# Kernel optimization log

Hardware: AMD Instinct MI355X
Metric: run time of the kernel (lower is better)

The kernel has to match this reference:

```python
import jax, jax.numpy as jnp
import numpy as np

B, N, M, L, H = 32, 4096, 256, 128, 4
GAMMA = 2.0


def setup_inputs() -> dict:
    key = jax.random.key(0)
    kx, km, kv, ku, kw = jax.random.split(key, 5)
    x = jax.random.normal(kx, (B, N, M), dtype=jnp.float32)
    masks = (jax.random.uniform(km, (B, N)) > 0.3).astype(jnp.float32)
    # VarianceScaling(scale=0.1, fan_in, uniform) ~ small init; exact dist doesn't affect math
    V = jax.random.normal(kv, (H, M, L), dtype=jnp.float32) * 0.02
    U = jax.random.normal(ku, (H, M, L), dtype=jnp.float32) * 0.02
    w = jax.random.normal(kw, (H, L, 1), dtype=jnp.float32) * 0.05
    return {"x": x, "masks": masks, "V": V, "U": U, "w": w}


def reference(x, masks, V, U, w):
    # x: [B,N,M], masks: [B,N], V/U: [H,M,L], w: [H,L,1]
    m = masks[:, None, :, None]  # [B,1,N,1] broadcast over heads
    gated = jnp.tanh(jnp.einsum('bnm,hml->bhnl', x, V)) * jax.nn.sigmoid(
        jnp.einsum('bnm,hml->bhnl', x, U))          # [B,H,N,L]
    logits = jnp.einsum('bhnl,hl->bhn', gated, w[..., 0])[..., None]  # [B,H,N,1]
    a = m * logits                                   # masked logits (as in original)
    a = m * jnp.exp(a)                               # masked exp
    a = a / jnp.sum(a, axis=2, keepdims=True)        # softmax over instances
    ag = a ** GAMMA
    a = ag / jnp.sum(ag, axis=2, keepdims=True)      # gamma-power renorm
    emb = jnp.einsum('bhnk,bnm->bhm', a, x)          # weighted sum; k is the trailing 1
    emb = emb.reshape(B, H * M)                      # concat heads along axis=1
    att = jnp.transpose(a, (1, 0, 2, 3))             # [H,B,N,1] (per-head attention list)
    return (att, emb)
```

## Files before the change

### kernel.cpp

```cpp
#include <hip/hip_runtime.h>
#include <hip/hip_bf16.h>
#include <stdint.h>

#define B_ 32
#define N_ 4096
#define M_ 256
#define L_ 128
#define H_ 4
#define BN_ (B_ * N_)

typedef __bf16 bf16x8 __attribute__((ext_vector_type(8)));
typedef float  f32x4  __attribute__((ext_vector_type(4)));

__device__ __forceinline__ unsigned short f2bf(float f) {
    unsigned int u = __float_as_uint(f);
    u += 0x7fffu + ((u >> 16) & 1u);
    return (unsigned short)(u >> 16);
}
__device__ __forceinline__ unsigned int pack2(float lo, float hi) {
    return (unsigned int)f2bf(lo) | ((unsigned int)f2bf(hi) << 16);
}

__global__ void prep_vu(const float* __restrict__ V, const float* __restrict__ U,
                        unsigned short* __restrict__ Vt, unsigned short* __restrict__ Ut) {
    int idx = blockIdx.x * 256 + threadIdx.x;
    int m = idx & (M_ - 1);
    int l = (idx >> 8) & (L_ - 1);
    int h = idx >> 15;
    Vt[idx] = f2bf(V[((size_t)h * M_ + m) * L_ + l]);
    Ut[idx] = f2bf(U[((size_t)h * M_ + m) * L_ + l]);
}

#define BM 128
#define BK 64

__global__ __launch_bounds__(256, 2)
void gemm_logits(const float* __restrict__ x,
                 const unsigned short* __restrict__ Vt,
                 const unsigned short* __restrict__ Ut,
                 const float* __restrict__ w,
                 float* __restrict__ logits) {
    __shared__ __align__(16) unsigned short xs[BM * BK];
    __shared__ __align__(16) unsigned short vs[L_ * BK];
    __shared__ __align__(16) unsigned short us[L_ * BK];
    __shared__ float wl[L_];

    const int h    = blockIdx.x >> 10;
    const int tile = blockIdx.x & 1023;
    const int row0 = tile * BM;
    const int tid  = threadIdx.x;
    const int lane = tid & 63;
    const int wave = tid >> 6;

    if (tid < L_) wl[tid] = w[h * L_ + tid];

    f32x4 accV[2][8], accU[2][8];
#pragma unroll
    for (int rf = 0; rf < 2; ++rf)
#pragma unroll
        for (int cf = 0; cf < 8; ++cf) {
            accV[rf][cf] = (f32x4){0.f, 0.f, 0.f, 0.f};
            accU[rf][cf] = (f32x4){0.f, 0.f, 0.f, 0.f};
        }

    const unsigned short* Vh = Vt + (size_t)h * L_ * M_;
    const unsigned short* Uh = Ut + (size_t)h * L_ * M_;

    const int g = lane >> 4;
    const int c = lane & 15;

    for (int ks = 0; ks < 4; ++ks) {
        const int k0 = ks * BK;
        __syncthreads();

#pragma unroll
        for (int p = 0; p < 4; ++p) {
            int row = p * 32 + (tid >> 3);
            int kk  = (tid & 7) * 8;
            const float* gx = x + (size_t)(row0 + row) * M_ + k0 + kk;
            float4 a = *(const float4*)gx;
            float4 b = *(const float4*)(gx + 4);
            uint4 o;
            o.x = pack2(a.x, a.y); o.y = pack2(a.z, a.w);
            o.z = pack2(b.x, b.y); o.w = pack2(b.z, b.w);
            int byte = (row * BK + kk) * 2;
            byte ^= (row & 7) << 4;
            *(uint4*)((char*)xs + byte) = o;
        }
#pragma unroll
        for (int p = 0; p < 4; ++p) {
            int l  = p * 32 + (tid >> 3);
            int kk = (tid & 7) * 8;
            uint4 v = *(const uint4*)(Vh + (size_t)l * M_ + k0 + kk);
            uint4 u = *(const uint4*)(Uh + (size_t)l * M_ + k0 + kk);
            int byte = (l * BK + kk) * 2;
            byte ^= (l & 7) << 4;
            *(uint4*)((char*)vs + byte) = v;
            *(uint4*)((char*)us + byte) = u;
        }
        __syncthreads();

#pragma unroll
        for (int ksub = 0; ksub < 2; ++ksub) {
            bf16x8 afr[2];
#pragma unroll
            for (int rf = 0; rf < 2; ++rf) {
                int row = wave * 32 + rf * 16 + c;
                int byte = (row * BK + ksub * 32 + g * 8) * 2;
                byte ^= (row & 7) << 4;
                afr[rf] = *(const bf16x8*)((const char*)xs + byte);
            }
#pragma unroll
            for (int cf = 0; cf < 8; ++cf) {
                int l = cf * 16 + c;
                int byte = (l * BK + ksub * 32 + g * 8) * 2;
                byte ^= (l & 7) << 4;
                bf16x8 bv = *(const bf16x8*)((const char*)vs + byte);
                bf16x8 bu = *(const bf16x8*)((const char*)us + byte);
#pragma unroll
                for (int rf = 0; rf < 2; ++rf) {
                    accV[rf][cf] = __builtin_amdgcn_mfma_f32_16x16x32_bf16(afr[rf], bv, accV[rf][cf], 0, 0, 0);
                    accU[rf][cf] = __builtin_amdgcn_mfma_f32_16x16x32_bf16(afr[rf], bu, accU[rf][cf], 0, 0, 0);
                }
            }
        }
    }

#pragma unroll
    for (int rf = 0; rf < 2; ++rf) {
        float plog[4] = {0.f, 0.f, 0.f, 0.f};
#pragma unroll
        for (int cf = 0; cf < 8; ++cf) {
            float wv = wl[cf * 16 + c];
#pragma unroll
            for (int i = 0; i < 4; ++i) {
                float vv = accV[rf][cf][i];
                float uu = accU[rf][cf][i];
                vv = fminf(fmaxf(vv, -20.f), 20.f);
                float e2v = __expf(2.f * vv);
                float t = __fdividef(e2v - 1.f, e2v + 1.f);
                float s = __fdividef(1.f, 1.f + __expf(-uu));
                plog[i] += t * s * wv;
            }
        }
#pragma unroll
        for (int i = 0; i < 4; ++i) {
            float v = plog[i];
            v += __shfl_xor(v, 1);
            v += __shfl_xor(v, 2);
            v += __shfl_xor(v, 4);
            v += __shfl_xor(v, 8);
            if (c == 0) {
                int rowflat = row0 + wave * 32 + rf * 16 + g * 4 + i;
                int b = rowflat >> 12;
                int n = rowflat & (N_ - 1);
                logits[((size_t)b * H_ + h) * N_ + n] = v;
            }
        }
    }
}

__global__ __launch_bounds__(256)
void softmax_att(const float* __restrict__ logits, const float* __restrict__ masks,
                 float* __restrict__ att) {
    const int bh = blockIdx.x;
    const int b = bh >> 2, h = bh & 3;
    __shared__ float e2s[N_];
    __shared__ float red[4];
    const int tid = threadIdx.x;

    float sum = 0.f;
#pragma unroll
    for (int i = 0; i < N_ / 256; ++i) {
        int n = i * 256 + tid;
        float lg = logits[((size_t)b * H_ + h) * N_ + n];
        float mv = masks[(size_t)b * N_ + n];
        float e = mv * __expf(mv * lg);
        float e2 = e * e;
        e2s[n] = e2;
        sum += e2;
    }
#pragma unroll
    for (int off = 32; off >= 1; off >>= 1) sum += __shfl_xor(sum, off);
    if ((tid & 63) == 0) red[tid >> 6] = sum;
    __syncthreads();
    float S = red[0] + red[1] + red[2] + red[3];
    float inv = 1.f / S;
#pragma unroll
    for (int i = 0; i < N_ / 256; ++i) {
        int n = i * 256 + tid;
        att[((size_t)h * B_ + b) * N_ + n] = e2s[n] * inv;
    }
}

#define NCH 32
#define CHUNK (N_ / NCH)

__global__ __launch_bounds__(256)
void emb_partial(const float* __restrict__ x, const float* __restrict__ att,
                 float* __restrict__ part) {
    const int bc = blockIdx.x;
    const int b = bc >> 5, ch = bc & 31;
    __shared__ float as[H_][CHUNK];
    const int tid = threadIdx.x;

    for (int i = tid; i < H_ * CHUNK; i += 256) {
        int hh = i >> 7;
        int j  = i & (CHUNK - 1);
        as[hh][j] = att[((size_t)hh * B_ + b) * N_ + ch * CHUNK + j];
    }
    __syncthreads();

    float a0 = 0.f, a1 = 0.f, a2 = 0.f, a3 = 0.f;
    const float* xp = x + ((size_t)b * N_ + ch * CHUNK) * M_ + tid;
#pragma unroll 4
    for (int j = 0; j < CHUNK; ++j) {
        float xv = xp[(size_t)j * M_];
        a0 += as[0][j] * xv;
        a1 += as[1][j] * xv;
        a2 += as[2][j] * xv;
        a3 += as[3][j] * xv;
    }
    float* pp = part + (size_t)bc * H_ * M_ + tid;
    pp[0 * M_] = a0; pp[1 * M_] = a1; pp[2 * M_] = a2; pp[3 * M_] = a3;
}

__global__ __launch_bounds__(256)
void emb_reduce(const float* __restrict__ part, float* __restrict__ emb) {
    int idx = blockIdx.x * 256 + threadIdx.x;
    int b = idx >> 10;
    int r = idx & 1023;
    float s = 0.f;
#pragma unroll
    for (int ci = 0; ci < NCH; ++ci)
        s += part[((size_t)(b * NCH + ci)) * (H_ * M_) + r];
    emb[idx] = s;
}

extern "C" void kernel_launch(void* const* d_in, const int* in_sizes, int n_in,
                              void* d_out, int out_size, void* d_ws, size_t ws_size,
                              hipStream_t stream) {
    const float* x     = (const float*)d_in[0];
    const float* masks = (const float*)d_in[1];
    const float* V     = (const float*)d_in[2];
    const float* U     = (const float*)d_in[3];
    const float* w     = (const float*)d_in[4];

    float* att = (float*)d_out;
    float* emb = att + (size_t)H_ * B_ * N_;

    char* ws = (char*)d_ws;
    unsigned short* Vt = (unsigned short*)ws;
    unsigned short* Ut = (unsigned short*)(ws + 262144);
    float* logits      = (float*)(ws + 524288);
    float* part        = (float*)(ws + 524288 + 2097152);

    prep_vu   <<<(H_ * L_ * M_) / 256, 256, 0, stream>>>(V, U, Vt, Ut);
    gemm_logits<<<(BN_ / BM) * H_,      256, 0, stream>>>(x, Vt, Ut, w, logits);
    softmax_att<<<B_ * H_,              256, 0, stream>>>(logits, masks, att);
    emb_partial<<<B_ * NCH,             256, 0, stream>>>(x, att, part);
    emb_reduce <<<(B_ * H_ * M_) / 256, 256, 0, stream>>>(part, emb);
}
```

Baseline: 186.9 us.

## Pre-convert x to swizzled bf16 tiles and stream them into LDS

```diff
diff --git a/kernel.cpp b/kernel.cpp
--- a/kernel.cpp
+++ b/kernel.cpp
@@ -11,6 +11,7 @@
 
 typedef __bf16 bf16x8 __attribute__((ext_vector_type(8)));
 typedef float  f32x4  __attribute__((ext_vector_type(4)));
+typedef float  f32x16 __attribute__((ext_vector_type(16)));
 
 __device__ __forceinline__ unsigned short f2bf(float f) {
     unsigned int u = __float_as_uint(f);
@@ -21,8 +22,197 @@
     return (unsigned int)f2bf(lo) | ((unsigned int)f2bf(hi) << 16);
 }
 
-__global__ void prep_vu(const float* __restrict__ V, const float* __restrict__ U,
-                        unsigned short* __restrict__ Vt, unsigned short* __restrict__ Ut) {
+__device__ __forceinline__ void gload16(const void* g, void* l) {
+    __builtin_amdgcn_global_load_lds(
+        (const __attribute__((address_space(1))) unsigned int*)g,
+        (__attribute__((address_space(3))) unsigned int*)l, 16, 0, 0);
+}
+
+__global__ void prep_x(const float* __restrict__ x, unsigned short* __restrict__ xb) {
+    const int blk  = blockIdx.x;
+    const int tile = blk >> 2, ks = blk & 3;
+    const int i    = threadIdx.x;
+    const int kk   = (i & 7) * 8;
+    char* dst = (char*)xb + (size_t)blk * 16384;
+#pragma unroll
+    for (int rep = 0; rep < 4; ++rep) {
+        int row = rep * 32 + (i >> 3);
+        const float* gx = x + (size_t)(tile * 128 + row) * M_ + ks * 64 + kk;
+        float4 a = *(const float4*)gx;
+        float4 b = *(const float4*)(gx + 4);
+        uint4 o;
+        o.x = pack2(a.x, a.y); o.y = pack2(a.z, a.w);
+        o.z = pack2(b.x, b.y); o.w = pack2(b.z, b.w);
+        int byte = (row * 64 + kk) * 2;
+        byte ^= (row & 7) << 4;
+        *(uint4*)(dst + byte) = o;
+    }
+}
+
+__global__ void prep_vu_img(const float* __restrict__ V, const float* __restrict__ U,
+                            unsigned short* __restrict__ vu) {
+    __shared__ float slab[64][129];
+    const int b   = blockIdx.x;
+    const int mat = b & 1, ks = (b >> 1) & 3, h = b >> 3;
+    const float* src = (mat ? U : V) + ((size_t)h * M_ + ks * 64) * L_;
+    const int tid = threadIdx.x;
+#pragma unroll
+    for (int rep = 0; rep < 32; ++rep) {
+        int idx = rep * 256 + tid;
+        slab[idx >> 7][idx & 127] = src[(size_t)(idx >> 7) * L_ + (idx & 127)];
+    }
+    __syncthreads();
+    char* dst = (char*)vu + (size_t)b * 16384;
+#pragma unroll
+    for (int rep = 0; rep < 4; ++rep) {
+        int cidx = rep * 256 + tid;
+        int l  = cidx >> 3;
+        int kk = (cidx & 7) * 8;
+        uint4 o;
+        o.x = pack2(slab[kk + 0][l], slab[kk + 1][l]);
+        o.y = pack2(slab[kk + 2][l], slab[kk + 3][l]);
+        o.z = pack2(slab[kk + 4][l], slab[kk + 5][l]);
+        o.w = pack2(slab[kk + 6][l], slab[kk + 7][l]);
+        int byte = (l * 64 + kk) * 2;
+        byte ^= (l & 7) << 4;
+        *(uint4*)(dst + byte) = o;
+    }
+}
+
+__global__ __launch_bounds__(256, 2)
+void gemm_fast(const unsigned short* __restrict__ xb,
+               const unsigned short* __restrict__ vu,
+               const float* __restrict__ w,
+               float* __restrict__ logits) {
+    __shared__ __align__(16) unsigned short xs[8192];
+    __shared__ __align__(16) unsigned short vs[8192];
+    __shared__ __align__(16) unsigned short us[8192];
+    __shared__ float wl[L_];
+    __shared__ float part[2][128];
+
+    const int orig    = blockIdx.x;
+    const int logical = (orig & 7) * 512 + (orig >> 3);
+    const int tile    = logical >> 2;
+    const int h       = logical & 3;
+
+    const int tid  = threadIdx.x;
+    const int lane = tid & 63;
+    const int wv   = tid >> 6;
+    const int cc   = lane & 31;
+    const int hi   = lane >> 5;
+    const int r0   = (wv & 1) * 64;
+    const int L0   = (wv >> 1) * 64;
+
+    if (tid < L_) wl[tid] = w[h * L_ + tid];
+
+    f32x16 accV[2][2], accU[2][2];
+#pragma unroll
+    for (int rf = 0; rf < 2; ++rf)
+#pragma unroll
+        for (int j = 0; j < 2; ++j) {
+            accV[rf][j] = (f32x16)(0.f);
+            accU[rf][j] = (f32x16)(0.f);
+        }
+
+    const char* xsrc0 = (const char*)xb + (size_t)tile * 4 * 16384;
+    const char* vusrc = (const char*)vu + (size_t)h * 4 * 32768;
+
+    for (int ks = 0; ks < 4; ++ks) {
+        if (ks) __syncthreads();
+        const char* xsrc = xsrc0 + ks * 16384;
+        const char* vsrc = vusrc + ks * 32768;
+        const char* usrc = vsrc + 16384;
+#pragma unroll
+        for (int j = 0; j < 4; ++j) {
+            int off = (wv * 4 + j) * 1024;
+            gload16(xsrc + off + lane * 16, (char*)xs + off);
+            gload16(vsrc + off + lane * 16, (char*)vs + off);
+            gload16(usrc + off + lane * 16, (char*)us + off);
+        }
+        __syncthreads();
+
+#pragma unroll
+        for (int ksub = 0; ksub < 4; ++ksub) {
+            const int kb = ksub * 32 + hi * 16;
+            bf16x8 a0, a1, bv0, bv1, bu0, bu1;
+            {
+                int r = r0 + cc;
+                int byte = (r * 128 + kb) ^ ((r & 7) << 4);
+                a0 = *(const bf16x8*)((const char*)xs + byte);
+                r = r0 + 32 + cc;
+                byte = (r * 128 + kb) ^ ((r & 7) << 4);
+                a1 = *(const bf16x8*)((const char*)xs + byte);
+                int l = L0 + cc;
+                byte = (l * 128 + kb) ^ ((l & 7) << 4);
+                bv0 = *(const bf16x8*)((const char*)vs + byte);
+                bu0 = *(const bf16x8*)((const char*)us + byte);
+                l = L0 + 32 + cc;
+                byte = (l * 128 + kb) ^ ((l & 7) << 4);
+                bv1 = *(const bf16x8*)((const char*)vs + byte);
+                bu1 = *(const bf16x8*)((const char*)us + byte);
+            }
+            accV[0][0] = __builtin_amdgcn_mfma_f32_32x32x16_bf16(a0, bv0, accV[0][0], 0, 0, 0);
+            accV[0][1] = __builtin_amdgcn_mfma_f32_32x32x16_bf16(a0, bv1, accV[0][1], 0, 0, 0);
+            accU[0][0] = __builtin_amdgcn_mfma_f32_32x32x16_bf16(a0, bu0, accU[0][0], 0, 0, 0);
+            accU[0][1] = __builtin_amdgcn_mfma_f32_32x32x16_bf16(a0, bu1, accU[0][1], 0, 0, 0);
+            accV[1][0] = __builtin_amdgcn_mfma_f32_32x32x16_bf16(a1, bv0, accV[1][0], 0, 0, 0);
+            accV[1][1] = __builtin_amdgcn_mfma_f32_32x32x16_bf16(a1, bv1, accV[1][1], 0, 0, 0);
+            accU[1][0] = __builtin_amdgcn_mfma_f32_32x32x16_bf16(a1, bu0, accU[1][0], 0, 0, 0);
+            accU[1][1] = __builtin_amdgcn_mfma_f32_32x32x16_bf16(a1, bu1, accU[1][1], 0, 0, 0);
+        }
+    }
+
+    const float w0 = wl[L0 + cc];
+    const float w1 = wl[L0 + 32 + cc];
+    float p[32];
+#pragma unroll
+    for (int rf = 0; rf < 2; ++rf)
+#pragma unroll
+        for (int i = 0; i < 16; ++i) {
+            float s = 0.f;
+#pragma unroll
+            for (int j = 0; j < 2; ++j) {
+                float vv = accV[rf][j][i];
+                float uu = accU[rf][j][i];
+                vv = fminf(fmaxf(vv, -20.f), 20.f);
+                float A = __expf(2.f * vv);
+                float E = __expf(fminf(-uu, 30.f));
+                float g = __fdividef(A - 1.f, (A + 1.f) * (1.f + E));
+                s += g * (j ? w1 : w0);
+            }
+            p[rf * 16 + i] = s;
+        }
+
+#pragma unroll
+    for (int st = 0; st < 5; ++st) {
+        const int m = 1 << st;
+        const int half = 16 >> st;
+#pragma unroll
+        for (int j = 0; j < half; ++j) {
+            float send = (cc & m) ? p[j] : p[j + half];
+            float recv = __shfl_xor(send, m, 64);
+            float keep = (cc & m) ? p[j + half] : p[j];
+            p[j] = keep + recv;
+        }
+    }
+    {
+        int slot = ((cc & 1) << 4) | ((cc & 2) << 2) | (cc & 4) | ((cc & 8) >> 2) | ((cc & 16) >> 4);
+        int rf = slot >> 4, i = slot & 15;
+        int rlocal = r0 + rf * 32 + (i & 3) + 8 * (i >> 2) + 4 * hi;
+        part[wv >> 1][rlocal] = p[0];
+    }
+    __syncthreads();
+    if (tid < 128) {
+        float v = part[0][tid] + part[1][tid];
+        int rowflat = tile * 128 + tid;
+        int b = rowflat >> 12;
+        int n = rowflat & (N_ - 1);
+        logits[((size_t)b * H_ + h) * N_ + n] = v;
+    }
+}
+
+__global__ void prep_vu_slow(const float* __restrict__ V, const float* __restrict__ U,
+                             unsigned short* __restrict__ Vt, unsigned short* __restrict__ Ut) {
     int idx = blockIdx.x * 256 + threadIdx.x;
     int m = idx & (M_ - 1);
     int l = (idx >> 8) & (L_ - 1);
@@ -65,14 +255,12 @@
 
     const unsigned short* Vh = Vt + (size_t)h * L_ * M_;
     const unsigned short* Uh = Ut + (size_t)h * L_ * M_;
-
     const int g = lane >> 4;
     const int c = lane & 15;
 
     for (int ks = 0; ks < 4; ++ks) {
         const int k0 = ks * BK;
         __syncthreads();
-
 #pragma unroll
         for (int p = 0; p < 4; ++p) {
             int row = p * 32 + (tid >> 3);
@@ -99,7 +287,6 @@
             *(uint4*)((char*)us + byte) = u;
         }
         __syncthreads();
-
 #pragma unroll
         for (int ksub = 0; ksub < 2; ++ksub) {
             bf16x8 afr[2];
@@ -125,13 +312,12 @@
             }
         }
     }
-
 #pragma unroll
     for (int rf = 0; rf < 2; ++rf) {
         float plog[4] = {0.f, 0.f, 0.f, 0.f};
 #pragma unroll
         for (int cf = 0; cf < 8; ++cf) {
-            float wv = wl[cf * 16 + c];
+            float wvv = wl[cf * 16 + c];
 #pragma unroll
             for (int i = 0; i < 4; ++i) {
                 float vv = accV[rf][cf][i];
@@ -140,7 +326,7 @@
                 float e2v = __expf(2.f * vv);
                 float t = __fdividef(e2v - 1.f, e2v + 1.f);
                 float s = __fdividef(1.f, 1.f + __expf(-uu));
-                plog[i] += t * s * wv;
+                plog[i] += t * s * wvv;
             }
         }
 #pragma unroll
@@ -250,14 +436,35 @@
     float* emb = att + (size_t)H_ * B_ * N_;
 
     char* ws = (char*)d_ws;
-    unsigned short* Vt = (unsigned short*)ws;
-    unsigned short* Ut = (unsigned short*)(ws + 262144);
-    float* logits      = (float*)(ws + 524288);
-    float* part        = (float*)(ws + 524288 + 2097152);
-
-    prep_vu   <<<(H_ * L_ * M_) / 256, 256, 0, stream>>>(V, U, Vt, Ut);
-    gemm_logits<<<(BN_ / BM) * H_,      256, 0, stream>>>(x, Vt, Ut, w, logits);
+    const size_t XB_BYTES  = (size_t)1024 * 4 * 16384;
+    const size_t VU_BYTES  = (size_t)32 * 16384;
+    const size_t LG_BYTES  = (size_t)B_ * H_ * N_ * 4;
+    const size_t PT_BYTES  = (size_t)B_ * NCH * H_ * M_ * 4;
+    const size_t NEED_FAST = XB_BYTES + VU_BYTES + LG_BYTES + PT_BYTES;
+
+    float* logits;
+    float* partp;
+
+    if (ws_size >= NEED_FAST) {
+        unsigned short* xb = (unsigned short*)ws;
+        unsigned short* vu = (unsigned short*)(ws + XB_BYTES);
+        logits = (float*)(ws + XB_BYTES + VU_BYTES);
+        partp  = (float*)(ws + XB_BYTES + VU_BYTES + LG_BYTES);
+
+        prep_x    <<<4096, 256, 0, stream>>>(x, xb);
+        prep_vu_img<<<32,  256, 0, stream>>>(V, U, vu);
+        gemm_fast <<<4096, 256, 0, stream>>>(xb, vu, w, logits);
+    } else {
+        unsigned short* Vt = (unsigned short*)ws;
+        unsigned short* Ut = (unsigned short*)(ws + 262144);
+        logits = (float*)(ws + 524288);
+        partp  = (float*)(ws + 524288 + LG_BYTES);
+
+        prep_vu_slow<<<512, 256, 0, stream>>>(V, U, Vt, Ut);
+        gemm_logits <<<4096, 256, 0, stream>>>(x, Vt, Ut, w, logits);
+    }
+
     softmax_att<<<B_ * H_,              256, 0, stream>>>(logits, masks, att);
-    emb_partial<<<B_ * NCH,             256, 0, stream>>>(x, att, part);
-    emb_reduce <<<(B_ * H_ * M_) / 256, 256, 0, stream>>>(part, emb);
-}
+    emb_partial<<<B_ * NCH,             256, 0, stream>>>(x, att, partp);
+    emb_reduce <<<(B_ * H_ * M_) / 256, 256, 0, stream>>>(partp, emb);
+}
```

Result: slower. 260.6 us (+39.4%).
